# Performance work log

Measured on AMD Instinct MI355X. Metric: run time of the kernel, lower is better.

The kernel has to match this reference:

```python
import jax, jax.numpy as jnp
import numpy as np

DIM = 512          # model dim
DH = 32            # dim_head
WSZ = 8            # window_size
HEADS = DIM // DH  # 16
INNER = HEADS * DH # 512
D4 = DIM // 4      # DPB hidden = 128
EPS = 1e-5


def _ln(x, g, b=None, eps=EPS):
    m = jnp.mean(x, axis=-1, keepdims=True)
    v = jnp.var(x, axis=-1, keepdims=True)
    y = (x - m) * jax.lax.rsqrt(v + eps) * g
    return y if b is None else y + b


def setup_inputs() -> dict:
    key = jax.random.key(0)
    ks = jax.random.split(key, 8)
    g = lambda k, shape, s=0.02: (jax.random.normal(k, shape, jnp.float32) * s)
    return {
        "x": jax.random.normal(ks[0], (16, 64, 64, DIM), jnp.float32),
        "norm_g": jnp.ones((DIM,), jnp.float32),
        "norm_b": jnp.zeros((DIM,), jnp.float32),
        "w_qkv": g(ks[1], (DIM, 3 * INNER)),
        "w_out": g(ks[2], (INNER, DIM)),
        "b_out": jnp.zeros((DIM,), jnp.float32),
        "dpb_w0": g(ks[3], (2, D4)), "dpb_b0": jnp.zeros((D4,), jnp.float32), "dpb_ln0": jnp.ones((D4,), jnp.float32),
        "dpb_w1": g(ks[4], (D4, D4)), "dpb_b1": jnp.zeros((D4,), jnp.float32), "dpb_ln1": jnp.ones((D4,), jnp.float32),
        "dpb_w2": g(ks[5], (D4, D4)), "dpb_b2": jnp.zeros((D4,), jnp.float32), "dpb_ln2": jnp.ones((D4,), jnp.float32),
        "dpb_w3": g(ks[6], (D4, 1)), "dpb_b3": jnp.zeros((1,), jnp.float32),
    }


def reference(x, norm_g, norm_b, w_qkv, w_out, b_out,
              dpb_w0, dpb_b0, dpb_ln0,
              dpb_w1, dpb_b1, dpb_ln1,
              dpb_w2, dpb_b2, dpb_ln2,
              dpb_w3, dpb_b3):
    B, H, W, d = x.shape
    w = WSZ
    scale = DH ** -0.5

    x = _ln(x, norm_g, norm_b)

    # 'short' attention: partition into non-overlapping wxw windows
    # b (h s1) (w s2) d -> (b h w) s1 s2 d
    xw = x.reshape(B, H // w, w, W // w, w, d).transpose(0, 1, 3, 2, 4, 5)
    xw = xw.reshape(-1, w, w, d)  # [nb, w, w, d]

    qkv = xw @ w_qkv  # 1x1 conv == dense, no bias
    q, k, v = jnp.split(qkv, 3, axis=-1)
    to_heads = lambda t: t.reshape(t.shape[0], w * w, HEADS, DH).transpose(0, 2, 1, 3)
    q, k, v = map(to_heads, (q, k, v))  # [nb, h, w*w, dh]

    sim = jnp.einsum('bhid,bhjd->bhij', q * scale, k)  # [nb, h, w*w, w*w]

    # relative-position gather indices (static)
    pos = jnp.arange(w)
    grid = jnp.stack(jnp.meshgrid(pos, pos, indexing='ij'), axis=-1).reshape(-1, 2)
    rel = grid[:, None] - grid[None, :] + (w - 1)
    rel_pos_indices = rel[..., 0] * (2 * w - 1) + rel[..., 1]  # [w*w, w*w]

    # dynamic position bias MLP over the (2w+1)^2 relative offsets
    p = jnp.arange(-w, w + 1)
    rp = jnp.stack(jnp.meshgrid(p, p, indexing='ij'), axis=-1).reshape(-1, 2).astype(jnp.float32)
    h = jax.nn.relu(_ln(rp @ dpb_w0 + dpb_b0, dpb_ln0))
    h = jax.nn.relu(_ln(h @ dpb_w1 + dpb_b1, dpb_ln1))
    h = jax.nn.relu(_ln(h @ dpb_w2 + dpb_b2, dpb_ln2))
    biases = (h @ dpb_w3 + dpb_b3)[:, 0]  # [(2w+1)^2]

    sim = sim + biases[rel_pos_indices]
    attn = jax.nn.softmax(sim, axis=-1)
    out = jnp.einsum('bhij,bhjd->bhid', attn, v)

    out = out.transpose(0, 2, 1, 3).reshape(-1, w, w, INNER)
    out = out @ w_out + b_out  # 1x1 conv with bias

    # (b h w) s1 s2 d -> b (h s1) (w s2) d
    out = out.reshape(B, H // w, W // w, w, w, d).transpose(0, 1, 3, 2, 4, 5)
    return out.reshape(B, H, W, d)
```

## Files before the change

### kernel.cpp

```cpp
#include <hip/hip_runtime.h>
#include <cstdint>
#include <cstddef>

typedef unsigned short u16;
typedef __attribute__((ext_vector_type(8))) short short8;
typedef __attribute__((ext_vector_type(4))) float f32x4;
typedef __attribute__((ext_vector_type(4))) unsigned short us4;

#define AS1 __attribute__((address_space(1)))
#define AS3 __attribute__((address_space(3)))

__device__ __forceinline__ u16 f2bf(float f) {
  union { float f; unsigned u; } v; v.f = f;
  unsigned r = v.u + 0x7fffu + ((v.u >> 16) & 1u);
  return (u16)(r >> 16);
}

__device__ __forceinline__ void gload_lds16(const u16* g, u16* l) {
  __builtin_amdgcn_global_load_lds((AS1 void*)g, (AS3 void*)l, 16, 0, 0);
}

__global__ void ln_cast_kernel(const float* __restrict__ x, const float* __restrict__ g,
                               const float* __restrict__ b, u16* __restrict__ out) {
  const int lane = threadIdx.x & 63;
  const int tok = blockIdx.x * 4 + (threadIdx.x >> 6);
  const float4* row = (const float4*)(x + (size_t)tok * 512);
  float4 v0 = row[lane];
  float4 v1 = row[lane + 64];
  float s = v0.x + v0.y + v0.z + v0.w + v1.x + v1.y + v1.z + v1.w;
  float q = v0.x*v0.x + v0.y*v0.y + v0.z*v0.z + v0.w*v0.w
          + v1.x*v1.x + v1.y*v1.y + v1.z*v1.z + v1.w*v1.w;
#pragma unroll
  for (int m = 1; m < 64; m <<= 1) { s += __shfl_xor(s, m, 64); q += __shfl_xor(q, m, 64); }
  const float mean = s * (1.0f / 512.0f);
  const float var = q * (1.0f / 512.0f) - mean * mean;
  const float r = rsqrtf(var + 1e-5f);
  const float4* g4 = (const float4*)g;
  const float4* b4 = (const float4*)b;
  float4 ga = g4[lane], gb = g4[lane + 64];
  float4 ba = b4[lane], bb = b4[lane + 64];
  us4 o0 = { f2bf((v0.x - mean) * r * ga.x + ba.x), f2bf((v0.y - mean) * r * ga.y + ba.y),
             f2bf((v0.z - mean) * r * ga.z + ba.z), f2bf((v0.w - mean) * r * ga.w + ba.w) };
  us4 o1 = { f2bf((v1.x - mean) * r * gb.x + bb.x), f2bf((v1.y - mean) * r * gb.y + bb.y),
             f2bf((v1.z - mean) * r * gb.z + bb.z), f2bf((v1.w - mean) * r * gb.w + bb.w) };
  *(us4*)(out + (size_t)tok * 512 + lane * 4) = o0;
  *(us4*)(out + (size_t)tok * 512 + 256 + lane * 4) = o1;
}

__global__ void prep_w_kernel(const float* __restrict__ wqkv, const float* __restrict__ wout,
                              u16* __restrict__ wqkvT, u16* __restrict__ woutT) {
  int idx = blockIdx.x * blockDim.x + threadIdx.x;
  if (idx < 512 * 1536) {
    int n = idx >> 9, k = idx & 511;
    wqkvT[idx] = f2bf(wqkv[k * 1536 + n]);
  } else {
    int j = idx - 512 * 1536;
    if (j < 512 * 512) {
      int n = j >> 9, k = j & 511;
      woutT[j] = f2bf(wout[k * 512 + n]);
    }
  }
}

__device__ __forceinline__ float lnrelu128(float a, float g, float* red, int tid) {
  float s = a, q = a * a;
#pragma unroll
  for (int m = 1; m < 64; m <<= 1) { s += __shfl_xor(s, m, 64); q += __shfl_xor(q, m, 64); }
  __syncthreads();
  if ((tid & 63) == 0) { red[tid >> 6] = s; red[2 + (tid >> 6)] = q; }
  __syncthreads();
  float S = red[0] + red[1], Q = red[2] + red[3];
  float mean = S * (1.f / 128.f);
  float var = Q * (1.f / 128.f) - mean * mean;
  float y = (a - mean) * rsqrtf(var + 1e-5f) * g;
  return fmaxf(y, 0.f);
}

__global__ void dpb_mlp_kernel(const float* __restrict__ w0, const float* __restrict__ b0, const float* __restrict__ g0,
                               const float* __restrict__ w1, const float* __restrict__ b1, const float* __restrict__ g1,
                               const float* __restrict__ w2, const float* __restrict__ b2, const float* __restrict__ g2,
                               const float* __restrict__ w3, const float* __restrict__ b3,
                               float* __restrict__ biases) {
  __shared__ float h[128];
  __shared__ float red[4];
  const int tid = threadIdx.x;
  const int row = blockIdx.x;
  const float p0 = (float)(row / 17) - 8.0f;
  const float p1 = (float)(row % 17) - 8.0f;
  float a = p0 * w0[tid] + p1 * w0[128 + tid] + b0[tid];
  a = lnrelu128(a, g0[tid], red, tid);
  h[tid] = a;
  __syncthreads();
  float acc = b1[tid];
  for (int i = 0; i < 128; ++i) acc += h[i] * w1[i * 128 + tid];
  acc = lnrelu128(acc, g1[tid], red, tid);
  h[tid] = acc;
  __syncthreads();
  float acc2 = b2[tid];
  for (int i = 0; i < 128; ++i) acc2 += h[i] * w2[i * 128 + tid];
  acc2 = lnrelu128(acc2, g2[tid], red, tid);
  float t = acc2 * w3[tid];
#pragma unroll
  for (int m = 1; m < 64; m <<= 1) t += __shfl_xor(t, m, 64);
  __syncthreads();
  if ((tid & 63) == 0) red[tid >> 6] = t;
  __syncthreads();
  if (tid == 0) biases[row] = red[0] + red[1] + b3[0];
}

__global__ void dpb_table_kernel(const float* __restrict__ biases, float* __restrict__ table) {
  int t = blockIdx.x * blockDim.x + threadIdx.x;
  if (t < 4096) {
    int i = t >> 6, j = t & 63;
    int r0 = (i >> 3) - (j >> 3) + 7;
    int r1 = (i & 7) - (j & 7) + 7;
    table[t] = biases[r0 * 15 + r1];
  }
}

template <int CT, bool F32OUT>
__global__ __launch_bounds__(256, 4) void gemm_bk64_kernel(const u16* __restrict__ A, const u16* __restrict__ BT,
                                                           void* __restrict__ Cv, const float* __restrict__ bias) {
  __shared__ __align__(16) u16 As[128 * 64];
  __shared__ __align__(16) u16 Bs[128 * 64];
  const int tid = threadIdx.x;
  const int w = tid >> 6, l = tid & 63;
  const int wr = w >> 1, wc = w & 1;
  const int cr = l & 15, cg = l >> 4;
  const int hcr = (cr + ((cr >> 3) << 2)) & 7;

  const int hw = blockIdx.x;
  const int ix = hw >> 3;
  const int rt = (hw & 7) + 8 * (ix / CT);
  const int ct = ix % CT;
  const size_t brow = (size_t)rt * 128;
  const size_t bcol = (size_t)ct * 128;
  const int N = CT * 128;

  const int srow8 = tid >> 3;
  const int hsrc = ((srow8 & 15) + (((srow8 >> 3) & 1) << 2)) & 7;
  const int csrc = ((tid & 7) ^ hsrc) * 8;
  const u16* gA = A + (brow + srow8) * 512 + csrc;
  const u16* gB = BT + (bcol + srow8) * 512 + csrc;

  const f32x4 zero = {0.f, 0.f, 0.f, 0.f};
  f32x4 acc[4][4];
#pragma unroll
  for (int i = 0; i < 4; ++i)
#pragma unroll
    for (int j = 0; j < 4; ++j) acc[i][j] = zero;

  const u16* aP = &As[(wr * 64 + cr) * 64];
  const u16* bP = &Bs[(wc * 64 + cr) * 64];

  for (int k0 = 0; k0 < 512; k0 += 64) {
#pragma unroll
    for (int j = 0; j < 4; ++j) {
      gload_lds16(gA + (size_t)j * 32 * 512 + k0, &As[j * 2048 + w * 512]);
      gload_lds16(gB + (size_t)j * 32 * 512 + k0, &Bs[j * 2048 + w * 512]);
    }
    __syncthreads();
#pragma unroll
    for (int ks = 0; ks < 2; ++ks) {
      short8 af[4], bf[4];
      const int pco = ((ks * 4 + cg) ^ hcr) * 8;
#pragma unroll
      for (int fr = 0; fr < 4; ++fr) af[fr] = *(const short8*)(aP + fr * 1024 + pco);
#pragma unroll
      for (int fc = 0; fc < 4; ++fc) bf[fc] = *(const short8*)(bP + fc * 1024 + pco);
#pragma unroll
      for (int fr = 0; fr < 4; ++fr)
#pragma unroll
        for (int fc = 0; fc < 4; ++fc)
          acc[fr][fc] = __builtin_amdgcn_mfma_f32_16x16x32_bf16(bf[fc], af[fr], acc[fr][fc], 0, 0, 0);
    }
    __syncthreads();
  }

  if (F32OUT) {
    float* C = (float*)Cv;
#pragma unroll
    for (int fc = 0; fc < 4; ++fc) {
      size_t col = bcol + wc * 64 + fc * 16 + cg * 4;
      float4 bv = *(const float4*)&bias[col];
#pragma unroll
      for (int fr = 0; fr < 4; ++fr) {
        size_t r = brow + wr * 64 + fr * 16 + cr;
        float4 o = { acc[fr][fc][0] + bv.x, acc[fr][fc][1] + bv.y,
                     acc[fr][fc][2] + bv.z, acc[fr][fc][3] + bv.w };
        *(float4*)(C + r * N + col) = o;
      }
    }
  } else {
    u16* C = (u16*)Cv;
#pragma unroll
    for (int fc = 0; fc < 4; ++fc) {
      size_t col = bcol + wc * 64 + fc * 16 + cg * 4;
#pragma unroll
      for (int fr = 0; fr < 4; ++fr) {
        size_t r = brow + wr * 64 + fr * 16 + cr;
        uint2 p;
        p.x = (unsigned)f2bf(acc[fr][fc][0]) | ((unsigned)f2bf(acc[fr][fc][1]) << 16);
        p.y = (unsigned)f2bf(acc[fr][fc][2]) | ((unsigned)f2bf(acc[fr][fc][3]) << 16);
        *(uint2*)(C + r * N + col) = p;
      }
    }
  }
}

__global__ __launch_bounds__(256, 3) void attn_kernel(const u16* __restrict__ qkv,
                                                      const float* __restrict__ table,
                                                      u16* __restrict__ aout) {
  __shared__ __align__(16) u16 VT[4][32 * 74];
  const int l = threadIdx.x & 63;
  const int wv = threadIdx.x >> 6;
  const int pair = blockIdx.x * 4 + wv;
  const int head = pair & 15;
  const int win = pair >> 4;
  const int base = ((win >> 6) << 12) + (((win >> 3) & 7) << 9) + ((win & 7) << 3);
  const int cr = l & 15, cg = l >> 4;
  u16* vt = VT[wv];

  short8 qf[4], kf[4], vl[4];
#pragma unroll
  for (int i = 0; i < 4; ++i) {
    int t = i * 16 + cr;
    size_t row = base + ((t >> 3) << 6) + (t & 7);
    const u16* rp = qkv + row * 1536 + head * 32 + cg * 8;
    qf[i] = *(const short8*)(rp);
    kf[i] = *(const short8*)(rp + 512);
    vl[i] = *(const short8*)(rp + 1024);
  }
  float4 tb[4][1];
  float4 tbl[4];
#pragma unroll
  for (int nt = 0; nt < 4; ++nt) tbl[nt] = *(const float4*)&table[(nt * 16 + cr) * 64 + 0 * 16 + cg * 4];

#pragma unroll
  for (int mt = 0; mt < 4; ++mt)
#pragma unroll
    for (int j = 0; j < 8; ++j)
      vt[(cg * 8 + j) * 74 + mt * 16 + cr] = (u16)vl[mt][j];

  const f32x4 zero = {0.f, 0.f, 0.f, 0.f};
  f32x4 s[4][4];
  __builtin_amdgcn_s_setprio(1);
#pragma unroll
  for (int mt = 0; mt < 4; ++mt)
#pragma unroll
    for (int nt = 0; nt < 4; ++nt)
      s[mt][nt] = __builtin_amdgcn_mfma_f32_16x16x32_bf16(kf[mt], qf[nt], zero, 0, 0, 0);
  __builtin_amdgcn_s_setprio(0);

  asm volatile("s_waitcnt lgkmcnt(0)" ::: "memory");
  __builtin_amdgcn_sched_barrier(0);
  short8 vfT[2][2];
#pragma unroll
  for (int dt = 0; dt < 2; ++dt)
#pragma unroll
    for (int kk = 0; kk < 2; ++kk)
      vfT[dt][kk] = *(const short8*)&vt[(dt * 16 + cr) * 74 + kk * 32 + cg * 8];

  const float scale = 0.17677669529663689f;
  f32x4 o[2][4];
#pragma unroll
  for (int dt = 0; dt < 2; ++dt)
#pragma unroll
    for (int nt = 0; nt < 4; ++nt) o[dt][nt] = zero;

  const int laneA = cr + 32 * (cg & 1);
  const int hi = cg >> 1;

#pragma unroll
  for (int nt = 0; nt < 4; ++nt) {
    float p[16];
    float mx = -3.0e38f;
#pragma unroll
    for (int mt = 0; mt < 4; ++mt) {
      float4 tbv = (mt == 0) ? tbl[nt] : *(const float4*)&table[(nt * 16 + cr) * 64 + mt * 16 + cg * 4];
      p[mt * 4 + 0] = s[mt][nt][0] * scale + tbv.x;
      p[mt * 4 + 1] = s[mt][nt][1] * scale + tbv.y;
      p[mt * 4 + 2] = s[mt][nt][2] * scale + tbv.z;
      p[mt * 4 + 3] = s[mt][nt][3] * scale + tbv.w;
      mx = fmaxf(mx, fmaxf(fmaxf(p[mt * 4], p[mt * 4 + 1]), fmaxf(p[mt * 4 + 2], p[mt * 4 + 3])));
    }
    mx = fmaxf(mx, __shfl_xor(mx, 16, 64));
    mx = fmaxf(mx, __shfl_xor(mx, 32, 64));
    float sum = 0.f;
#pragma unroll
    for (int i = 0; i < 16; ++i) { p[i] = __expf(p[i] - mx); sum += p[i]; }
    sum += __shfl_xor(sum, 16, 64);
    sum += __shfl_xor(sum, 32, 64);
    const float inv = 1.0f / sum;

    unsigned pk[4][2];
#pragma unroll
    for (int mt = 0; mt < 4; ++mt)
#pragma unroll
      for (int i = 0; i < 2; ++i)
        pk[mt][i] = (unsigned)f2bf(p[mt * 4 + 2 * i] * inv) | ((unsigned)f2bf(p[mt * 4 + 2 * i + 1] * inv) << 16);

#pragma unroll
    for (int kk = 0; kk < 2; ++kk) {
      union { unsigned u[4]; short8 v; } pf;
#pragma unroll
      for (int i = 0; i < 2; ++i) {
        unsigned x0 = (unsigned)__shfl((int)pk[2 * kk][i], laneA, 64);
        unsigned x1 = (unsigned)__shfl((int)pk[2 * kk + 1][i], laneA, 64);
        unsigned y0 = (unsigned)__shfl((int)pk[2 * kk][i], laneA + 16, 64);
        unsigned y1 = (unsigned)__shfl((int)pk[2 * kk + 1][i], laneA + 16, 64);
        pf.u[i] = hi ? x1 : x0;
        pf.u[2 + i] = hi ? y1 : y0;
      }
      __builtin_amdgcn_s_setprio(1);
#pragma unroll
      for (int dt = 0; dt < 2; ++dt)
        o[dt][nt] = __builtin_amdgcn_mfma_f32_16x16x32_bf16(vfT[dt][kk], pf.v, o[dt][nt], 0, 0, 0);
      __builtin_amdgcn_s_setprio(0);
    }
  }

#pragma unroll
  for (int nt = 0; nt < 4; ++nt) {
    int t = nt * 16 + cr;
    size_t row = base + ((t >> 3) << 6) + (t & 7);
#pragma unroll
    for (int dt = 0; dt < 2; ++dt) {
      uint2 pck;
      pck.x = (unsigned)f2bf(o[dt][nt][0]) | ((unsigned)f2bf(o[dt][nt][1]) << 16);
      pck.y = (unsigned)f2bf(o[dt][nt][2]) | ((unsigned)f2bf(o[dt][nt][3]) << 16);
      *(uint2*)(aout + row * 512 + head * 32 + dt * 16 + cg * 4) = pck;
    }
  }
}

extern "C" void kernel_launch(void* const* d_in, const int* in_sizes, int n_in,
                              void* d_out, int out_size, void* d_ws, size_t ws_size,
                              hipStream_t stream) {
  const float* x = (const float*)d_in[0];
  const float* norm_g = (const float*)d_in[1];
  const float* norm_b = (const float*)d_in[2];
  const float* w_qkv = (const float*)d_in[3];
  const float* w_out = (const float*)d_in[4];
  const float* b_out = (const float*)d_in[5];
  const float* dw0 = (const float*)d_in[6];
  const float* db0 = (const float*)d_in[7];
  const float* dg0 = (const float*)d_in[8];
  const float* dw1 = (const float*)d_in[9];
  const float* db1 = (const float*)d_in[10];
  const float* dg1 = (const float*)d_in[11];
  const float* dw2 = (const float*)d_in[12];
  const float* db2 = (const float*)d_in[13];
  const float* dg2 = (const float*)d_in[14];
  const float* dw3 = (const float*)d_in[15];
  const float* db3 = (const float*)d_in[16];

  char* ws = (char*)d_ws;
  size_t off = 0;
  auto take = [&](size_t bytes) { char* p = ws + off; off += (bytes + 255) & ~(size_t)255; return p; };
  u16* xln = (u16*)take(65536ull * 512 * 2);
  u16* wqkvT = (u16*)take(1536 * 512 * 2);
  u16* woutT = (u16*)take(512 * 512 * 2);
  float* biases = (float*)take(289 * 4);
  float* table = (float*)take(4096 * 4);

  ln_cast_kernel<<<16384, 256, 0, stream>>>(x, norm_g, norm_b, xln);
  prep_w_kernel<<<4096, 256, 0, stream>>>(w_qkv, w_out, wqkvT, woutT);
  dpb_mlp_kernel<<<289, 128, 0, stream>>>(dw0, db0, dg0, dw1, db1, dg1, dw2, db2, dg2, dw3, db3, biases);
  dpb_table_kernel<<<16, 256, 0, stream>>>(biases, table);

  size_t rem = (ws_size > off) ? ws_size - off : 0;
  int nch = 4;
  if (rem >= 32768ull * 2048 * 2 + 512) nch = 2;
  const int rows = 65536 / nch;
  u16* qkvbuf = (u16*)take((size_t)rows * 1536 * 2);
  u16* attnbuf = (u16*)take((size_t)rows * 512 * 2);

  for (int c = 0; c < nch; ++c) {
    const u16* Ac = xln + (size_t)c * rows * 512;
    gemm_bk64_kernel<12, false><<<(rows / 128) * 12, 256, 0, stream>>>(Ac, wqkvT, (void*)qkvbuf, nullptr);
    attn_kernel<<<(rows / 64) * 16 / 4, 256, 0, stream>>>(qkvbuf, table, attnbuf);
    float* Cc = (float*)d_out + (size_t)c * rows * 512;
    gemm_bk64_kernel<4, true><<<(rows / 128) * 4, 256, 0, stream>>>(attnbuf, woutT, (void*)Cc, b_out);
  }
}
```

Measured before the change: 339.5 us.

## Interleave QK MFMA, softmax and PV per query tile in attn kernel

Restructures the window attention kernel so the QK^T MFMAs, softmax, PV MFMAs and output store are done per 16-query tile inside one loop, instead of computing all 16 score tiles up front and holding all 8 output accumulators. This cuts live accumulator registers (from 64+32 floats to 16+8), which should ease register pressure and help the launch_bounds occupancy target. It also drops the table preload and loads bias values inside the loop. The cost is less independent MFMA work in flight between dependent steps, and interleaved global stores.

```diff
diff --git a/kernel.cpp b/kernel.cpp
--- a/kernel.cpp
+++ b/kernel.cpp
@@ -221,36 +221,24 @@
   const int cr = l & 15, cg = l >> 4;
   u16* vt = VT[wv];
 
-  short8 qf[4], kf[4], vl[4];
-#pragma unroll
-  for (int i = 0; i < 4; ++i) {
-    int t = i * 16 + cr;
-    size_t row = base + ((t >> 3) << 6) + (t & 7);
-    const u16* rp = qkv + row * 1536 + head * 32 + cg * 8;
-    qf[i] = *(const short8*)(rp);
-    kf[i] = *(const short8*)(rp + 512);
-    vl[i] = *(const short8*)(rp + 1024);
-  }
-  float4 tb[4][1];
-  float4 tbl[4];
-#pragma unroll
-  for (int nt = 0; nt < 4; ++nt) tbl[nt] = *(const float4*)&table[(nt * 16 + cr) * 64 + 0 * 16 + cg * 4];
-
-#pragma unroll
-  for (int mt = 0; mt < 4; ++mt)
-#pragma unroll
-    for (int j = 0; j < 8; ++j)
-      vt[(cg * 8 + j) * 74 + mt * 16 + cr] = (u16)vl[mt][j];
-
-  const f32x4 zero = {0.f, 0.f, 0.f, 0.f};
-  f32x4 s[4][4];
-  __builtin_amdgcn_s_setprio(1);
-#pragma unroll
-  for (int mt = 0; mt < 4; ++mt)
-#pragma unroll
-    for (int nt = 0; nt < 4; ++nt)
-      s[mt][nt] = __builtin_amdgcn_mfma_f32_16x16x32_bf16(kf[mt], qf[nt], zero, 0, 0, 0);
-  __builtin_amdgcn_s_setprio(0);
+  short8 qf[4], kf[4];
+  {
+    short8 vl[4];
+#pragma unroll
+    for (int i = 0; i < 4; ++i) {
+      int t = i * 16 + cr;
+      size_t row = base + ((t >> 3) << 6) + (t & 7);
+      const u16* rp = qkv + row * 1536 + head * 32 + cg * 8;
+      qf[i] = *(const short8*)(rp);
+      kf[i] = *(const short8*)(rp + 512);
+      vl[i] = *(const short8*)(rp + 1024);
+    }
+#pragma unroll
+    for (int mt = 0; mt < 4; ++mt)
+#pragma unroll
+      for (int j = 0; j < 8; ++j)
+        vt[(cg * 8 + j) * 74 + mt * 16 + cr] = (u16)vl[mt][j];
+  }
 
   asm volatile("s_waitcnt lgkmcnt(0)" ::: "memory");
   __builtin_amdgcn_sched_barrier(0);
@@ -261,27 +249,29 @@
     for (int kk = 0; kk < 2; ++kk)
       vfT[dt][kk] = *(const short8*)&vt[(dt * 16 + cr) * 74 + kk * 32 + cg * 8];
 
+  const f32x4 zero = {0.f, 0.f, 0.f, 0.f};
   const float scale = 0.17677669529663689f;
-  f32x4 o[2][4];
-#pragma unroll
-  for (int dt = 0; dt < 2; ++dt)
-#pragma unroll
-    for (int nt = 0; nt < 4; ++nt) o[dt][nt] = zero;
-
   const int laneA = cr + 32 * (cg & 1);
   const int hi = cg >> 1;
 
 #pragma unroll
   for (int nt = 0; nt < 4; ++nt) {
+    f32x4 s4[4];
+    __builtin_amdgcn_s_setprio(1);
+#pragma unroll
+    for (int mt = 0; mt < 4; ++mt)
+      s4[mt] = __builtin_amdgcn_mfma_f32_16x16x32_bf16(kf[mt], qf[nt], zero, 0, 0, 0);
+    __builtin_amdgcn_s_setprio(0);
+
     float p[16];
     float mx = -3.0e38f;
 #pragma unroll
     for (int mt = 0; mt < 4; ++mt) {
-      float4 tbv = (mt == 0) ? tbl[nt] : *(const float4*)&table[(nt * 16 + cr) * 64 + mt * 16 + cg * 4];
-      p[mt * 4 + 0] = s[mt][nt][0] * scale + tbv.x;
-      p[mt * 4 + 1] = s[mt][nt][1] * scale + tbv.y;
-      p[mt * 4 + 2] = s[mt][nt][2] * scale + tbv.z;
-      p[mt * 4 + 3] = s[mt][nt][3] * scale + tbv.w;
+      float4 tb = *(const float4*)&table[(nt * 16 + cr) * 64 + mt * 16 + cg * 4];
+      p[mt * 4 + 0] = s4[mt][0] * scale + tb.x;
+      p[mt * 4 + 1] = s4[mt][1] * scale + tb.y;
+      p[mt * 4 + 2] = s4[mt][2] * scale + tb.z;
+      p[mt * 4 + 3] = s4[mt][3] * scale + tb.w;
       mx = fmaxf(mx, fmaxf(fmaxf(p[mt * 4], p[mt * 4 + 1]), fmaxf(p[mt * 4 + 2], p[mt * 4 + 3])));
     }
     mx = fmaxf(mx, __shfl_xor(mx, 16, 64));
@@ -300,6 +290,7 @@
       for (int i = 0; i < 2; ++i)
         pk[mt][i] = (unsigned)f2bf(p[mt * 4 + 2 * i] * inv) | ((unsigned)f2bf(p[mt * 4 + 2 * i + 1] * inv) << 16);
 
+    f32x4 o2[2] = {zero, zero};
 #pragma unroll
     for (int kk = 0; kk < 2; ++kk) {
       union { unsigned u[4]; short8 v; } pf;
@@ -315,20 +306,17 @@
       __builtin_amdgcn_s_setprio(1);
 #pragma unroll
       for (int dt = 0; dt < 2; ++dt)
-        o[dt][nt] = __builtin_amdgcn_mfma_f32_16x16x32_bf16(vfT[dt][kk], pf.v, o[dt][nt], 0, 0, 0);
+        o2[dt] = __builtin_amdgcn_mfma_f32_16x16x32_bf16(vfT[dt][kk], pf.v, o2[dt], 0, 0, 0);
       __builtin_amdgcn_s_setprio(0);
     }
-  }
-
-#pragma unroll
-  for (int nt = 0; nt < 4; ++nt) {
+
     int t = nt * 16 + cr;
     size_t row = base + ((t >> 3) << 6) + (t & 7);
 #pragma unroll
     for (int dt = 0; dt < 2; ++dt) {
       uint2 pck;
-      pck.x = (unsigned)f2bf(o[dt][nt][0]) | ((unsigned)f2bf(o[dt][nt][1]) << 16);
-      pck.y = (unsigned)f2bf(o[dt][nt][2]) | ((unsigned)f2bf(o[dt][nt][3]) << 16);
+      pck.x = (unsigned)f2bf(o2[dt][0]) | ((unsigned)f2bf(o2[dt][1]) << 16);
+      pck.y = (unsigned)f2bf(o2[dt][2]) | ((unsigned)f2bf(o2[dt][3]) << 16);
       *(uint2*)(aout + row * 512 + head * 32 + dt * 16 + cg * 4) = pck;
     }
   }
```

Result: no change. 335.0 us (-1.3%).
